# Kernel optimization log

Measured on AMD Instinct MI355X. Metric: run time of the kernel, lower is better.

Reference implementation:

```python
import jax, jax.numpy as jnp
import numpy as np
from functools import partial

B, S, T = 32, 64, 64
VS, VT = 32000, 32000
E, H = 256, 512            # embed_dim, encoder hidden per direction
DH = 2 * H                 # decoder hidden (= encoder_hidden_dim)
A = 128                    # attention_dim


def _p(key, shape, scale=0.05):
    return scale * jax.random.normal(key, shape, dtype=jnp.float32)


def setup_inputs() -> dict:
    key = jax.random.key(0)
    ks = jax.random.split(key, 32)
    inp = {
        'src': jax.random.randint(ks[0], (B, S), 0, VS),
        'tgt_input': jax.random.randint(ks[1], (B, T), 0, VT),
        # encoder
        'enc_emb': _p(ks[2], (VS, E)),
        'enc_Wih_f': _p(ks[3], (4 * H, E)), 'enc_Whh_f': _p(ks[4], (4 * H, H)),
        'enc_bih_f': _p(ks[5], (4 * H,)),  'enc_bhh_f': _p(ks[6], (4 * H,)),
        'enc_Wih_b': _p(ks[7], (4 * H, E)), 'enc_Whh_b': _p(ks[8], (4 * H, H)),
        'enc_bih_b': _p(ks[9], (4 * H,)),  'enc_bhh_b': _p(ks[10], (4 * H,)),
        # decoder
        'dec_emb': _p(ks[11], (VT, E)),
        'Wd': _p(ks[12], (A, DH)), 'bd': _p(ks[13], (A,)),
        'We': _p(ks[14], (A, DH)), 'be': _p(ks[15], (A,)),
        'v_att': _p(ks[16], (A,)), 'bv': _p(ks[17], ()),
        'dec_Wih': _p(ks[18], (4 * DH, E + DH)), 'dec_Whh': _p(ks[19], (4 * DH, DH)),
        'dec_bih': _p(ks[20], (4 * DH,)), 'dec_bhh': _p(ks[21], (4 * DH,)),
        'Wo': _p(ks[22], (VT, DH + DH)), 'bo': _p(ks[23], (VT,)),
    }
    return inp


def _lstm_cell(x, h, c, Wih, Whh, b):
    g = x @ Wih.T + h @ Whh.T + b
    i, f, gg, o = jnp.split(g, 4, axis=-1)  # PyTorch gate order: i,f,g,o
    i, f, o = jax.nn.sigmoid(i), jax.nn.sigmoid(f), jax.nn.sigmoid(o)
    c_new = f * c + i * jnp.tanh(gg)
    h_new = o * jnp.tanh(c_new)
    return h_new, c_new


def _lstm_scan(xs, Wih, Whh, b, reverse):
    # xs: [S,B,E] -> outputs [S,B,H] aligned with input positions, final (h,c)
    h0 = jnp.zeros((xs.shape[1], Whh.shape[1]), xs.dtype)
    def step(carry, x):
        h, c = carry
        h, c = _lstm_cell(x, h, c, Wih, Whh, b)
        return (h, c), h
    (hT, cT), hs = jax.lax.scan(step, (h0, h0), xs, reverse=reverse)
    return hs, hT, cT


def _forward(src, tgt_input, enc_emb,
             enc_Wih_f, enc_Whh_f, enc_bih_f, enc_bhh_f,
             enc_Wih_b, enc_Whh_b, enc_bih_b, enc_bhh_b,
             dec_emb, Wd, bd, We, be, v_att, bv,
             dec_Wih, dec_Whh, dec_bih, dec_bhh, Wo, bo):
    # ---- Encoder: bidirectional single-layer LSTM ----
    emb = enc_emb[src]                              # [B,S,E]
    xs = emb.transpose(1, 0, 2)                     # [S,B,E]
    hs_f, hT_f, cT_f = _lstm_scan(xs, enc_Wih_f, enc_Whh_f, enc_bih_f + enc_bhh_f, False)
    hs_b, hT_b, cT_b = _lstm_scan(xs, enc_Wih_b, enc_Whh_b, enc_bih_b + enc_bhh_b, True)
    enc_out = jnp.concatenate([hs_f, hs_b], axis=-1).transpose(1, 0, 2)  # [B,S,2H]
    h = jnp.concatenate([hT_f, hT_b], axis=-1)      # [B,DH]
    c = jnp.concatenate([cT_f, cT_b], axis=-1)

    # ---- Decoder with Bahdanau attention (full teacher forcing) ----
    enc_proj = enc_out @ We.T + be                  # [B,S,A] precomputed
    dec_b = dec_bih + dec_bhh
    tgt_emb = dec_emb[tgt_input].transpose(1, 0, 2)  # [T,B,E]

    def dec_step(carry, emb_t):
        h, c = carry
        dproj = h @ Wd.T + bd                       # [B,A]
        energy = jnp.tanh(dproj[:, None, :] + enc_proj)  # [B,S,A]
        scores = energy @ v_att + bv                # [B,S]
        w = jax.nn.softmax(scores, axis=1)
        ctx = jnp.einsum('bs,bsh->bh', w, enc_out)  # [B,DH]
        x = jnp.concatenate([emb_t, ctx], axis=-1)  # [B,E+DH]
        h_new, c_new = _lstm_cell(x, h, c, dec_Wih, dec_Whh, dec_b)
        logits = jnp.concatenate([h_new, ctx], axis=-1) @ Wo.T + bo  # [B,VT]
        return (h_new, c_new), logits

    _, logits = jax.lax.scan(dec_step, (h, c), tgt_emb)  # [T,B,VT]
    return logits.transpose(1, 0, 2)                     # [B,T,VT]


def reference(src, tgt_input, enc_emb,
              enc_Wih_f, enc_Whh_f, enc_bih_f, enc_bhh_f,
              enc_Wih_b, enc_Whh_b, enc_bih_b, enc_bhh_b,
              dec_emb, Wd, bd, We, be, v_att, bv,
              dec_Wih, dec_Whh, dec_bih, dec_bhh, Wo, bo):
    return _forward(src, tgt_input, enc_emb,
                    enc_Wih_f, enc_Whh_f, enc_bih_f, enc_bhh_f,
                    enc_Wih_b, enc_Whh_b, enc_bih_b, enc_bhh_b,
                    dec_emb, Wd, bd, We, be, v_att, bv,
                    dec_Wih, dec_Whh, dec_bih, dec_bhh, Wo, bo)
```

## Files before the change

### kernel.cpp

```cpp
#include <hip/hip_runtime.h>


using u16 = unsigned short;
using u32 = unsigned int;
using u64 = unsigned long long;
using f32x4 = __attribute__((ext_vector_type(4))) float;
using s16x8 = __attribute__((ext_vector_type(8))) short;
using u16x4 = __attribute__((ext_vector_type(4))) unsigned short;

__device__ __forceinline__ float sigm_(float x) { return 1.0f / (1.0f + expf(-x)); }
__device__ __forceinline__ float tanh_(float x) {
    float e = __expf(fminf(2.0f * x, 30.0f));
    return (e - 1.0f) / (e + 1.0f);
}

__device__ __forceinline__ u16 f2bf(float x) {
    u32 u = __float_as_uint(x);
    u += 0x7fffu + ((u >> 16) & 1u);
    return (u16)(u >> 16);
}
__device__ __forceinline__ u32 pk2(float a, float b) {
    return (u32)f2bf(a) | ((u32)f2bf(b) << 16);
}
__device__ __forceinline__ float bf2f(u16 v) {
    return __uint_as_float((u32)v << 16);
}

__device__ __forceinline__ void ast32(u32* p, u32 v) {
    __hip_atomic_store(p, v, __ATOMIC_RELAXED, __HIP_MEMORY_SCOPE_AGENT);
}

#define MFMA __builtin_amdgcn_mfma_f32_16x16x32_bf16

#define GLL(g, l) __builtin_amdgcn_global_load_lds( \
    (__attribute__((address_space(1))) void*)(g),   \
    (__attribute__((address_space(3))) void*)(l), 16, 0, 0)

__device__ __forceinline__ void poll8(const int* go8) {
    if (threadIdx.x < 8) {
        const int* p = go8 + threadIdx.x * 16;
        while (__hip_atomic_load(p, __ATOMIC_RELAXED, __HIP_MEMORY_SCOPE_AGENT) == 0)
            __builtin_amdgcn_s_sleep(1);
    }
    __syncthreads();
    asm volatile("" ::: "memory");
}
__device__ __forceinline__ void arrive8(int* cnt8, int* go8, int line, int perline) {
    asm volatile("s_waitcnt vmcnt(0) lgkmcnt(0)" ::: "memory");
    __syncthreads();
    if (threadIdx.x == 0) {
        int old = __hip_atomic_fetch_add(cnt8 + line * 16, 1, __ATOMIC_RELAXED,
                                         __HIP_MEMORY_SCOPE_AGENT);
        if (old == perline - 1)
            __hip_atomic_store(go8 + line * 16, 1, __ATOMIC_RELAXED, __HIP_MEMORY_SCOPE_AGENT);
    }
}

__global__ __launch_bounds__(256) void k_zero(float* __restrict__ p, int n) {
    int i = blockIdx.x * 256 + threadIdx.x;
    if (i < n) p[i] = 0.0f;
}

__global__ __launch_bounds__(256) void k_cast_bf16(const float* __restrict__ in,
                                                   u16* __restrict__ outp, int n8) {
    int idx = blockIdx.x * 256 + threadIdx.x;
    if (idx >= n8) return;
    const f32x4* p = (const f32x4*)in + (size_t)idx * 2;
    f32x4 a = p[0], c = p[1];
    u32* o = (u32*)(outp + (size_t)idx * 8);
    o[0] = pk2(a.x, a.y); o[1] = pk2(a.z, a.w);
    o[2] = pk2(c.x, c.y); o[3] = pk2(c.z, c.w);
}

__global__ __launch_bounds__(256) void k_embed_bf(const int* __restrict__ tok,
                                                  const float* __restrict__ emb,
                                                  u16* __restrict__ outp) {
    int idx = blockIdx.x * 256 + threadIdx.x;
    int r = idx >> 6, e4 = idx & 63;
    int outer = r >> 5, b = r & 31;
    int tk = tok[b * 64 + outer];
    f32x4 v = ((const f32x4*)emb)[(size_t)tk * 64 + e4];
    u32* o = (u32*)(outp + (size_t)r * 256 + (e4 << 2));
    o[0] = pk2(v.x, v.y); o[1] = pk2(v.z, v.w);
}

__global__ __launch_bounds__(256) void k_prep_perm(
    const float* __restrict__ src, u16* __restrict__ dst,
    int J, int K4, int srcStride, int srcOff, int total)
{
    int idx = blockIdx.x * 256 + threadIdx.x;
    if (idx >= total) return;
    int n = idx / K4, kq = (idx - n * K4) << 2;
    int orig = (n & 3) * J + (n >> 2);
    f32x4 v = *(const f32x4*)(src + (size_t)orig * srcStride + srcOff + kq);
    u32* o = (u32*)(dst + (size_t)n * (K4 << 2) + kq);
    o[0] = pk2(v.x, v.y); o[1] = pk2(v.z, v.w);
}

__global__ __launch_bounds__(256) void k_prep_ws(
    const float* __restrict__ W, u16* __restrict__ dst)
{
    int idx = blockIdx.x * 256 + threadIdx.x;
    int n = idx >> 8, kp = idx & 255, k0 = kp << 1;
    int orig = (n & 3) * 512 + (n >> 2);
    const float* s = W + (size_t)orig * 512 + k0;
    int g = n >> 5, r = n & 31;
    int byteoff = (k0 << 1) ^ ((r & 7) << 4);
    *(u32*)((char*)dst + (size_t)g * 32768 + r * 1024 + byteoff) = pk2(s[0], s[1]);
}

__global__ __launch_bounds__(256) void k_prep_w2s(
    const float* __restrict__ Whh, const float* __restrict__ Wih, u16* __restrict__ dst)
{
    int idx = blockIdx.x * 256 + threadIdx.x;
    int n = idx >> 10, kp = idx & 1023, k0 = kp << 1;
    int orig = (n & 3) * 1024 + (n >> 2);
    const float* s = (k0 < 1024) ? (Whh + (size_t)orig * 1024 + k0)
                                 : (Wih + (size_t)orig * 1280 + 256 + (k0 - 1024));
    int g = n >> 5, r = n & 31;
    int byteoff = (k0 << 1) ^ ((r & 7) << 4);
    *(u32*)((char*)dst + (size_t)g * 131072 + r * 4096 + byteoff) = pk2(s[0], s[1]);
}

__global__ __launch_bounds__(256) void k_gemm_bf(
    const u16* __restrict__ A, const u16* __restrict__ B, int K,
    const float* __restrict__ b1, const float* __restrict__ b2, int biasJ,
    float* __restrict__ C, int ldc, int nM, int nN, int remapOut, int swz)
{
    __shared__ __align__(16) u16 As[128 * 32];
    __shared__ __align__(16) u16 Bs[128 * 32];
    int w = blockIdx.x;
    if (swz) { int cpx = (nM * nN) >> 3; w = (w & 7) * cpx + (w >> 3); }
    int bm = (w % nM) * 128, bn = (w / nM) * 128;
    int tid = threadIdx.x, wave = tid >> 6, lane = tid & 63;
    int wm = wave & 1, wn = wave >> 1;
    f32x4 acc[4][4] = {};

    int rA = wave * 32 + (lane >> 2);
    int cb2 = (lane & 3) * 16;
    const char* gA = (const char*)A + ((size_t)(bm + rA) * K) * 2 + cb2;
    const char* gB = (const char*)B + ((size_t)(bn + rA) * K) * 2 + cb2;
    size_t rowskip = (size_t)16 * K * 2;
    char* lA = (char*)As + wave * 2048;
    char* lB = (char*)Bs + wave * 2048;
    const u16* rdA = As + (wm * 64 + (lane & 15)) * 32 + (lane >> 4) * 8;
    const u16* rdB = Bs + (wn * 64 + (lane & 15)) * 32 + (lane >> 4) * 8;

    for (int k0 = 0; k0 < K; k0 += 32) {
        size_t kb = (size_t)k0 * 2;
        GLL(gA + kb, lA); GLL(gA + kb + rowskip, lA + 1024);
        GLL(gB + kb, lB); GLL(gB + kb + rowskip, lB + 1024);
        __syncthreads();
        s16x8 af[4], bfv[4];
#pragma unroll
        for (int m2 = 0; m2 < 4; ++m2) af[m2] = *(const s16x8*)(rdA + m2 * 512);
#pragma unroll
        for (int n2 = 0; n2 < 4; ++n2) bfv[n2] = *(const s16x8*)(rdB + n2 * 512);
#pragma unroll
        for (int m2 = 0; m2 < 4; ++m2)
#pragma unroll
            for (int n2 = 0; n2 < 4; ++n2)
                acc[m2][n2] = MFMA(af[m2], bfv[n2], acc[m2][n2], 0, 0, 0);
        __syncthreads();
    }

    int rbase = bm + wm * 64 + ((lane >> 4) << 2);
    int cbase = bn + wn * 64 + (lane & 15);
#pragma unroll
    for (int n2 = 0; n2 < 4; ++n2) {
        int col = cbase + n2 * 16;
        int bcol = biasJ ? ((col & 3) * biasJ + (col >> 2)) : col;
        float bias = (b1 ? b1[bcol] : 0.0f) + (b2 ? b2[bcol] : 0.0f);
#pragma unroll
        for (int m2 = 0; m2 < 4; ++m2) {
            f32x4 v = acc[m2][n2];
#pragma unroll
            for (int jj = 0; jj < 4; ++jj) {
                int row = rbase + m2 * 16 + jj;
                int orow = remapOut ? ((row & 31) * 64 + (row >> 5)) : row;
                C[(size_t)orow * ldc + col] = v[jj] + bias;
            }
        }
    }
}

__global__ __launch_bounds__(256, 1) void k_enc_persist(
    const u16* __restrict__ Wsf, const u16* __restrict__ Wsb,
    const float* __restrict__ Gfp, const float* __restrict__ Gbp,
    u16* __restrict__ henc,
    float* __restrict__ cfb,
    u16* __restrict__ encbf,
    int* __restrict__ cnt8, int* __restrict__ go8)
{
    __shared__ __align__(16) char smem[50176];
    int tid = threadIdx.x, lane = tid & 63, q = tid >> 6;
    int dir = blockIdx.x >> 6, g = blockIdx.x & 63;
    const char* wsrc = (const char*)(dir ? Wsb : Wsf) + (size_t)g * 32768;
#pragma unroll
    for (int it = 0; it < 8; ++it)
        GLL(wsrc + it * 4096 + tid * 16, smem + it * 4096 + tid * 16);
    __syncthreads();

    float* sacc = (float*)(smem + 32768);
    u16* hst = (u16*)(smem + 49664);
    const float* Gp = dir ? Gbp : Gfp;
    float* cB = cfb + dir * 16384;
    int lr = lane & 15, lk = (lane >> 4) << 3;
    int bb = tid & 31, jl = tid >> 5;
    int n0 = g * 32, j = g * 8 + jl;

    for (int s = 0; s < 64; ++s) {
        if (s) poll8(go8 + s * 128);
        int t = dir ? (63 - s) : s;
        f32x4 p4 = *(const f32x4*)(Gp + ((size_t)(t * 32 + bb)) * 2048 + n0 + (jl << 2));
        const u16* hA = henc + (size_t)s * 32768 + dir * 16384;
        s16x8 afr[8];
#pragma unroll
        for (int it = 0; it < 4; ++it) {
            int ke = q * 128 + it * 32 + lk;
            afr[2 * it]     = *(const s16x8*)(hA + lr * 512 + ke);
            afr[2 * it + 1] = *(const s16x8*)(hA + (lr + 16) * 512 + ke);
        }
        f32x4 acc00 = {}, acc01 = {}, acc10 = {}, acc11 = {};
#pragma unroll
        for (int it = 0; it < 4; ++it) {
            int ke = q * 128 + it * 32 + lk;
            int kb = ke << 1;
            s16x8 b0 = *(const s16x8*)(smem + lr * 1024 + (kb ^ ((lr & 7) << 4)));
            int r1 = lr + 16;
            s16x8 b1 = *(const s16x8*)(smem + r1 * 1024 + (kb ^ ((r1 & 7) << 4)));
            acc00 = MFMA(afr[2 * it], b0, acc00, 0, 0, 0);
            acc01 = MFMA(afr[2 * it], b1, acc01, 0, 0, 0);
            acc10 = MFMA(afr[2 * it + 1], b0, acc10, 0, 0, 0);
            acc11 = MFMA(afr[2 * it + 1], b1, acc11, 0, 0, 0);
        }
        int rw = (lane >> 4) << 2;
#pragma unroll
        for (int rr = 0; rr < 4; ++rr) {
            sacc[q * 1056 + (rw + rr) * 33 + lr]        = acc00[rr];
            sacc[q * 1056 + (rw + rr) * 33 + 16 + lr]   = acc01[rr];
            sacc[q * 1056 + (16 + rw + rr) * 33 + lr]      = acc10[rr];
            sacc[q * 1056 + (16 + rw + rr) * 33 + 16 + lr] = acc11[rr];
        }
        __syncthreads();
        {
            int c4 = jl << 2;
            float gi = 0, gf = 0, gg = 0, go2 = 0;
#pragma unroll
            for (int q2 = 0; q2 < 4; ++q2) {
                const float* sp = sacc + q2 * 1056 + bb * 33 + c4;
                gi += sp[0]; gf += sp[1]; gg += sp[2]; go2 += sp[3];
            }
            gi += p4.x; gf += p4.y; gg += p4.z; go2 += p4.w;
            float* cp = cB + bb * 512 + j;
            float cn = sigm_(gf) * cp[0] + sigm_(gi) * tanhf(gg);
            cp[0] = cn;
            float h = sigm_(go2) * tanhf(cn);
            u16 h16 = f2bf(h);
            encbf[((size_t)(bb * 64 + t)) * 1024 + dir * 512 + j] = h16;
            hst[bb * 8 + jl] = h16;
        }
        __syncthreads();
        if (tid < 128) {
            int bb2 = tid >> 2, p2 = tid & 3;
            u32 wv = (u32)hst[bb2 * 8 + 2 * p2] | ((u32)hst[bb2 * 8 + 2 * p2 + 1] << 16);
            ast32((u32*)(henc + (size_t)(s + 1) * 32768 + dir * 16384) + bb2 * 256 + g * 4 + p2, wv);
        }
        arrive8(cnt8 + (s + 1) * 128, go8 + (s + 1) * 128, blockIdx.x & 7, 16);
    }
}

__global__ __launch_bounds__(256) void k_dec_init(
    const u16* __restrict__ henc, const float* __restrict__ cfb,
    u16* __restrict__ hcarr, float* __restrict__ cd)
{
    int idx = blockIdx.x * 256 + threadIdx.x;
    int b = idx >> 10, j = idx & 1023;
    int dir = (j >> 9), jj = j & 511;
    hcarr[b * 2048 + j] = henc[(size_t)64 * 32768 + dir * 16384 + b * 512 + jj];
    cd[b * 1024 + j] = cfb[dir * 16384 + b * 512 + jj];
}

__global__ __launch_bounds__(256, 1) void k_dec_persist(
    const u16* __restrict__ W2s, const u16* __restrict__ encbf,
    const float* __restrict__ Prep,
    const u16* __restrict__ Wd_bf, const float* __restrict__ bd,
    const float* __restrict__ eproj, const float* __restrict__ v_att,
    const float* __restrict__ bv,
    u16* __restrict__ hcarr, float* __restrict__ cd, u16* __restrict__ Abf,
    const u16* __restrict__ Wbf, const float* __restrict__ bo,
    float* __restrict__ outp,
    int* __restrict__ hCnt8, int* __restrict__ goH8,
    int* __restrict__ ctxCnt8, int* __restrict__ goCtx8)
{
    __shared__ __align__(16) char smem[148480];
    int blk = blockIdx.x, tid = threadIdx.x, lane = tid & 63, q = tid >> 6;

    if (blk >= 160) {
        int w = blk - 160;
        u16* As = (u16*)smem;
        u16* Bs = (u16*)(smem + 8192);
        int wave = q, wm = wave & 1, wn = wave >> 1;
        int rA = wave * 32 + (lane >> 2);
        int cb2 = (lane & 3) * 16;
        size_t rowskip = (size_t)16 * 2048 * 2;
        char* lA = (char*)As + wave * 2048;
        char* lB = (char*)Bs + wave * 2048;
        const u16* rdA = As + (wm * 64 + (lane & 15)) * 32 + (lane >> 4) * 8;
        const u16* rdB = Bs + (wn * 64 + (lane & 15)) * 32 + (lane >> 4) * 8;
        for (int g = 0; g < 16; ++g) {
            poll8(goH8 + (4 * g + 4) * 128);
            int bm = g * 128;
            const char* gA = (const char*)Abf + ((size_t)(bm + rA) * 2048) * 2 + cb2;
            for (int nt = w; nt < 250; nt += 96) {
                int bn = nt * 128;
                const char* gB = (const char*)Wbf + ((size_t)(bn + rA) * 2048) * 2 + cb2;
                f32x4 acc[4][4] = {};
                for (int k0 = 0; k0 < 2048; k0 += 32) {
                    size_t kb = (size_t)k0 * 2;
                    GLL(gA + kb, lA); GLL(gA + kb + rowskip, lA + 1024);
                    GLL(gB + kb, lB); GLL(gB + kb + rowskip, lB + 1024);
                    __syncthreads();
                    s16x8 af[4], bfv[4];
#pragma unroll
                    for (int m2 = 0; m2 < 4; ++m2) af[m2] = *(const s16x8*)(rdA + m2 * 512);
#pragma unroll
                    for (int n2 = 0; n2 < 4; ++n2) bfv[n2] = *(const s16x8*)(rdB + n2 * 512);
#pragma unroll
                    for (int m2 = 0; m2 < 4; ++m2)
#pragma unroll
                        for (int n2 = 0; n2 < 4; ++n2)
                            acc[m2][n2] = MFMA(af[m2], bfv[n2], acc[m2][n2], 0, 0, 0);
                    __syncthreads();
                }
                int rbase = bm + wm * 64 + ((lane >> 4) << 2);
                int cbase = bn + wn * 64 + (lane & 15);
#pragma unroll
                for (int n2 = 0; n2 < 4; ++n2) {
                    int col = cbase + n2 * 16;
                    float bias = bo[col];
#pragma unroll
                    for (int m2 = 0; m2 < 4; ++m2) {
                        f32x4 v = acc[m2][n2];
#pragma unroll
                        for (int jj = 0; jj < 4; ++jj) {
                            int row = rbase + m2 * 16 + jj;
                            int orow = (row & 31) * 64 + (row >> 5);
                            outp[(size_t)orow * 32000 + col] = v[jj] + bias;
                        }
                    }
                }
            }
        }
        return;
    }

    bool isgate = blk < 128;
    {
        const char* src = isgate ? ((const char*)W2s + (size_t)blk * 131072)
                                 : ((const char*)encbf + (size_t)(blk - 128) * 131072);
#pragma unroll
        for (int it = 0; it < 32; ++it)
            GLL(src + it * 4096 + tid * 16, smem + it * 4096 + tid * 16);
    }
    __syncthreads();

    float* sacc = (float*)(smem + 131072);
    u16* hst    = (u16*)(smem + 147968);
    float* hsh  = (float*)(smem + 131072);
    float* red  = (float*)(smem + 135168);
    float* dp   = (float*)(smem + 136192);
    float* sc   = (float*)(smem + 136704);

    int lr = lane & 15, lk = (lane >> 4) << 3;
    int bb = tid & 31, jl = tid >> 5;
    int n0 = blk * 32, j = blk * 8 + jl;
    int b = blk - 128;

    for (int t = 0; t < 64; ++t) {
        if (t) poll8(goH8 + t * 128);
        const u16* hcT = hcarr + (size_t)t * 65536;
        if (isgate) {
            f32x4 p4 = *(const f32x4*)(Prep + ((size_t)(t * 32 + bb)) * 4096 + n0 + (jl << 2));
            s16x8 afr[16];
#pragma unroll
            for (int it = 0; it < 8; ++it) {
                int ke = q * 256 + it * 32 + lk;
                afr[2 * it]     = *(const s16x8*)(hcT + lr * 2048 + ke);
                afr[2 * it + 1] = *(const s16x8*)(hcT + (lr + 16) * 2048 + ke);
            }
            f32x4 acc00 = {}, acc01 = {}, acc10 = {}, acc11 = {};
#pragma unroll
            for (int it = 0; it < 8; ++it) {
                int ke = q * 256 + it * 32 + lk;
                int kb = ke << 1;
                s16x8 b0 = *(const s16x8*)(smem + lr * 4096 + (kb ^ ((lr & 7) << 4)));
                int r1 = lr + 16;
                s16x8 b1 = *(const s16x8*)(smem + r1 * 4096 + (kb ^ ((r1 & 7) << 4)));
                acc00 = MFMA(afr[2 * it], b0, acc00, 0, 0, 0);
                acc01 = MFMA(afr[2 * it], b1, acc01, 0, 0, 0);
                acc10 = MFMA(afr[2 * it + 1], b0, acc10, 0, 0, 0);
                acc11 = MFMA(afr[2 * it + 1], b1, acc11, 0, 0, 0);
            }
            poll8(goCtx8 + t * 128);
#pragma unroll
            for (int it = 0; it < 8; ++it) {
                int ke = 1024 + q * 256 + it * 32 + lk;
                afr[2 * it]     = *(const s16x8*)(hcT + lr * 2048 + ke);
                afr[2 * it + 1] = *(const s16x8*)(hcT + (lr + 16) * 2048 + ke);
            }
#pragma unroll
            for (int it = 0; it < 8; ++it) {
                int ke = 1024 + q * 256 + it * 32 + lk;
                int kb = ke << 1;
                s16x8 b0 = *(const s16x8*)(smem + lr * 4096 + (kb ^ ((lr & 7) << 4)));
                int r1 = lr + 16;
                s16x8 b1 = *(const s16x8*)(smem + r1 * 4096 + (kb ^ ((r1 & 7) << 4)));
                acc00 = MFMA(afr[2 * it], b0, acc00, 0, 0, 0);
                acc01 = MFMA(afr[2 * it], b1, acc01, 0, 0, 0);
                acc10 = MFMA(afr[2 * it + 1], b0, acc10, 0, 0, 0);
                acc11 = MFMA(afr[2 * it + 1], b1, acc11, 0, 0, 0);
            }
            int rw = (lane >> 4) << 2;
#pragma unroll
            for (int rr = 0; rr < 4; ++rr) {
                sacc[q * 1056 + (rw + rr) * 33 + lr]        = acc00[rr];
                sacc[q * 1056 + (rw + rr) * 33 + 16 + lr]   = acc01[rr];
                sacc[q * 1056 + (16 + rw + rr) * 33 + lr]      = acc10[rr];
                sacc[q * 1056 + (16 + rw + rr) * 33 + 16 + lr] = acc11[rr];
            }
            __syncthreads();
            {
                int c4 = jl << 2;
                float gi = 0, gf = 0, gg = 0, go2 = 0;
#pragma unroll
                for (int q2 = 0; q2 < 4; ++q2) {
                    const float* sp = sacc + q2 * 1056 + bb * 33 + c4;
                    gi += sp[0]; gf += sp[1]; gg += sp[2]; go2 += sp[3];
                }
                gi += p4.x; gf += p4.y; gg += p4.z; go2 += p4.w;
                int ci = bb * 1024 + j;
                float cn = sigm_(gf) * cd[ci] + sigm_(gi) * tanhf(gg);
                cd[ci] = cn;
                float h = sigm_(go2) * tanhf(cn);
                hst[bb * 8 + jl] = f2bf(h);
            }
            __syncthreads();
            if (tid < 128) {
                int bb2 = tid >> 2, p2 = tid & 3;
                u32 wv = (u32)hst[bb2 * 8 + 2 * p2] | ((u32)hst[bb2 * 8 + 2 * p2 + 1] << 16);
                ast32((u32*)(hcarr + (size_t)(t + 1) * 65536) + bb2 * 1024 + blk * 4 + p2, wv);
                ast32((u32*)Abf + (size_t)(t * 32 + bb2) * 1024 + blk * 4 + p2, wv);
            }
            arrive8(hCnt8 + (t + 1) * 128, goH8 + (t + 1) * 128, blk & 7, 16);
        } else {
            {
                u16x4 hv = *(const u16x4*)(hcT + b * 2048 + (tid << 2));
                hsh[(tid << 2) + 0] = bf2f(hv.x);
                hsh[(tid << 2) + 1] = bf2f(hv.y);
                hsh[(tid << 2) + 2] = bf2f(hv.z);
                hsh[(tid << 2) + 3] = bf2f(hv.w);
            }
            __syncthreads();
            {
                int a = tid & 127, half = tid >> 7;
                const u16* wr = Wd_bf + ((size_t)a << 10) + (half << 9);
                const float* hh = hsh + (half << 9);
                float s0 = 0, s1 = 0, s2 = 0, s3 = 0;
#pragma unroll 4
                for (int k = 0; k < 512; k += 32) {
                    s16x8 w0 = *(const s16x8*)(wr + k);
                    s16x8 w1 = *(const s16x8*)(wr + k + 8);
                    s16x8 w2 = *(const s16x8*)(wr + k + 16);
                    s16x8 w3 = *(const s16x8*)(wr + k + 24);
#pragma unroll
                    for (int e = 0; e < 8; ++e) {
                        s0 += bf2f((u16)w0[e]) * hh[k + e];
                        s1 += bf2f((u16)w1[e]) * hh[k + 8 + e];
                        s2 += bf2f((u16)w2[e]) * hh[k + 16 + e];
                        s3 += bf2f((u16)w3[e]) * hh[k + 24 + e];
                    }
                }
                red[tid] = (s0 + s1) + (s2 + s3);
            }
            __syncthreads();
            if (tid < 128) dp[tid] = red[tid] + red[tid + 128] + bd[tid];
            __syncthreads();
            {
                int si = tid >> 2, qq = tid & 3;
                const float* ep = eproj + ((size_t)(b * 64 + si)) * 128 + qq * 32;
                float s = 0.0f;
#pragma unroll 8
                for (int a2 = 0; a2 < 32; ++a2)
                    s += v_att[qq * 32 + a2] * tanh_(dp[qq * 32 + a2] + ep[a2]);
                red[tid] = s;
            }
            __syncthreads();
            if (tid < 64) {
                float x = red[tid * 4] + red[tid * 4 + 1] + red[tid * 4 + 2] + red[tid * 4 + 3] + bv[0];
                float mx = x;
#pragma unroll
                for (int off = 32; off; off >>= 1) mx = fmaxf(mx, __shfl_xor(mx, off));
                float e = __expf(x - mx), ss = e;
#pragma unroll
                for (int off = 32; off; off >>= 1) ss += __shfl_xor(ss, off);
                sc[tid] = e / ss;
            }
            __syncthreads();
            {
                const u16* eL = (const u16*)smem;
                int c0i = tid << 2;
                float c0 = 0, c1 = 0, c2 = 0, c3 = 0;
                for (int s2 = 0; s2 < 64; ++s2) {
                    float wgt = sc[s2];
                    u16x4 rp = *(const u16x4*)(eL + s2 * 1024 + c0i);
                    c0 += wgt * bf2f(rp.x); c1 += wgt * bf2f(rp.y);
                    c2 += wgt * bf2f(rp.z); c3 += wgt * bf2f(rp.w);
                }
                u32 cw0 = pk2(c0, c1), cw1 = pk2(c2, c3);
                u32* hw = (u32*)hcT + b * 1024 + 512 + (tid << 1);
                ast32(hw, cw0); ast32(hw + 1, cw1);
                u32* aw = (u32*)(Abf + ((size_t)(t * 32 + b)) * 2048 + 1024 + c0i);
                ast32(aw, cw0); ast32(aw + 1, cw1);
            }
            arrive8(ctxCnt8 + t * 128, goCtx8 + t * 128, blk & 7, 4);
        }
    }
}

extern "C" void kernel_launch(void* const* d_in, const int* in_sizes, int n_in,
                              void* d_out, int out_size, void* d_ws, size_t ws_size,
                              hipStream_t stream)
{
    (void)in_sizes; (void)n_in; (void)out_size; (void)ws_size;
    const int*   src     = (const int*)d_in[0];
    const int*   tgt     = (const int*)d_in[1];
    const float* enc_emb = (const float*)d_in[2];
    const float* eWih_f  = (const float*)d_in[3];
    const float* eWhh_f  = (const float*)d_in[4];
    const float* ebih_f  = (const float*)d_in[5];
    const float* ebhh_f  = (const float*)d_in[6];
    const float* eWih_b  = (const float*)d_in[7];
    const float* eWhh_b  = (const float*)d_in[8];
    const float* ebih_b  = (const float*)d_in[9];
    const float* ebhh_b  = (const float*)d_in[10];
    const float* dec_emb = (const float*)d_in[11];
    const float* Wd      = (const float*)d_in[12];
    const float* bd      = (const float*)d_in[13];
    const float* We      = (const float*)d_in[14];
    const float* be      = (const float*)d_in[15];
    const float* v_att   = (const float*)d_in[16];
    const float* bv      = (const float*)d_in[17];
    const float* dWih    = (const float*)d_in[18];
    const float* dWhh    = (const float*)d_in[19];
    const float* dbih    = (const float*)d_in[20];
    const float* dbhh    = (const float*)d_in[21];
    const float* Wo      = (const float*)d_in[22];
    const float* bo      = (const float*)d_in[23];
    float* out = (float*)d_out;

    char* wp = (char*)d_ws;
    auto alloc = [&](size_t nbytes) -> void* {
        void* p = (void*)wp;
        wp += (nbytes + 255) & ~(size_t)255;
        return p;
    };
    u16*   Xe_bf = (u16*)alloc(2048u * 256 * 2);
    u16*   Ed_bf = (u16*)alloc(2048u * 256 * 2);
    float* Gf_p  = (float*)alloc(2048u * 2048 * 4);
    float* Gb_p  = (float*)alloc(2048u * 2048 * 4);
    float* Pre_p = (float*)alloc(2048u * 4096 * 4);
    float* zr    = (float*)alloc(329728u);
    float* cfb   = zr;
    char*  sy    = (char*)zr + 131072;
    int*   cntE8 = (int*)(sy);
    int*   goE8  = (int*)(sy + 33280);
    int*   hCnt8 = (int*)(sy + 66560);
    int*   goH8  = (int*)(sy + 99840);
    int*   ctxC8 = (int*)(sy + 133120);
    int*   goX8  = (int*)(sy + 165888);
    u16*   henc  = (u16*)alloc(65u * 32768 * 2);
    u16*   hcarr = (u16*)alloc(65u * 65536 * 2);
    u16*   encbf = (u16*)alloc(2048u * 1024 * 2);
    float* eproj = (float*)alloc(2048u * 128 * 4);
    float* cd    = (float*)alloc(32768u * 4);
    u16*   Abf   = (u16*)alloc(2048u * 2048 * 2);
    u16*   Wbf   = (u16*)alloc(32000u * 2048 * 2);
    u16*   W2s   = (u16*)alloc(4096u * 2048 * 2);
    u16*   Wsf   = (u16*)alloc(2048u * 512 * 2);
    u16*   Wsb   = (u16*)alloc(2048u * 512 * 2);
    u16*   Wembf = (u16*)alloc(2048u * 256 * 2);
    u16*   Wembb = (u16*)alloc(2048u * 256 * 2);
    u16*   Wembd = (u16*)alloc(4096u * 256 * 2);
    u16*   We_bf = (u16*)alloc(128u * 1024 * 2);
    u16*   Wd_bf = (u16*)alloc(128u * 1024 * 2);

    k_zero<<<322, 256, 0, stream>>>(zr, 82432);
    k_zero<<<64, 256, 0, stream>>>((float*)henc, 16384);

    k_cast_bf16<<<32000, 256, 0, stream>>>(Wo, Wbf, 8192000);
    k_cast_bf16<<<64, 256, 0, stream>>>(We, We_bf, 16384);
    k_cast_bf16<<<64, 256, 0, stream>>>(Wd, Wd_bf, 16384);
    k_prep_perm<<<512, 256, 0, stream>>>(eWih_f, Wembf, 512, 64, 256, 0, 131072);
    k_prep_perm<<<512, 256, 0, stream>>>(eWih_b, Wembb, 512, 64, 256, 0, 131072);
    k_prep_perm<<<1024, 256, 0, stream>>>(dWih, Wembd, 1024, 64, 1280, 0, 262144);
    k_prep_ws<<<2048, 256, 0, stream>>>(eWhh_f, Wsf);
    k_prep_ws<<<2048, 256, 0, stream>>>(eWhh_b, Wsb);
    k_prep_w2s<<<16384, 256, 0, stream>>>(dWhh, dWih, W2s);

    k_embed_bf<<<512, 256, 0, stream>>>(src, enc_emb, Xe_bf);
    k_embed_bf<<<512, 256, 0, stream>>>(tgt, dec_emb, Ed_bf);

    k_gemm_bf<<<256, 256, 0, stream>>>(Xe_bf, Wembf, 256, ebih_f, ebhh_f, 512,
                                       Gf_p, 2048, 16, 16, 0, 1);
    k_gemm_bf<<<256, 256, 0, stream>>>(Xe_bf, Wembb, 256, ebih_b, ebhh_b, 512,
                                       Gb_p, 2048, 16, 16, 0, 1);
    k_gemm_bf<<<512, 256, 0, stream>>>(Ed_bf, Wembd, 256, dbih, dbhh, 1024,
                                       Pre_p, 4096, 16, 32, 0, 1);

    k_enc_persist<<<128, 256, 0, stream>>>(Wsf, Wsb, Gf_p, Gb_p, henc, cfb, encbf,
                                           cntE8, goE8);

    k_gemm_bf<<<16, 256, 0, stream>>>(encbf, We_bf, 1024, be, nullptr, 0,
                                      eproj, 128, 16, 1, 0, 1);
    k_dec_init<<<128, 256, 0, stream>>>(henc, cfb, hcarr, cd);

    k_dec_persist<<<256, 256, 0, stream>>>(W2s, encbf, Pre_p, Wd_bf, bd, eproj,
                                           v_att, bv, hcarr, cd, Abf,
                                           Wbf, bo, out,
                                           hCnt8, goH8, ctxC8, goX8);
}
```

Measured before the change: 2.280 ms.

## Overlap weight bf16 casts with encoder recurrence and batch output GEMM per 256 rows

After: 2.272 ms. No clear change (-0.3%).

```diff
diff --git a/kernel.cpp b/kernel.cpp
--- a/kernel.cpp
+++ b/kernel.cpp
@@ -59,17 +59,6 @@
 __global__ __launch_bounds__(256) void k_zero(float* __restrict__ p, int n) {
     int i = blockIdx.x * 256 + threadIdx.x;
     if (i < n) p[i] = 0.0f;
-}
-
-__global__ __launch_bounds__(256) void k_cast_bf16(const float* __restrict__ in,
-                                                   u16* __restrict__ outp, int n8) {
-    int idx = blockIdx.x * 256 + threadIdx.x;
-    if (idx >= n8) return;
-    const f32x4* p = (const f32x4*)in + (size_t)idx * 2;
-    f32x4 a = p[0], c = p[1];
-    u32* o = (u32*)(outp + (size_t)idx * 8);
-    o[0] = pk2(a.x, a.y); o[1] = pk2(a.z, a.w);
-    o[2] = pk2(c.x, c.y); o[3] = pk2(c.z, c.w);
 }
 
 __global__ __launch_bounds__(256) void k_embed_bf(const int* __restrict__ tok,
@@ -107,19 +96,6 @@
     int g = n >> 5, r = n & 31;
     int byteoff = (k0 << 1) ^ ((r & 7) << 4);
     *(u32*)((char*)dst + (size_t)g * 32768 + r * 1024 + byteoff) = pk2(s[0], s[1]);
-}
-
-__global__ __launch_bounds__(256) void k_prep_w2s(
-    const float* __restrict__ Whh, const float* __restrict__ Wih, u16* __restrict__ dst)
-{
-    int idx = blockIdx.x * 256 + threadIdx.x;
-    int n = idx >> 10, kp = idx & 1023, k0 = kp << 1;
-    int orig = (n & 3) * 1024 + (n >> 2);
-    const float* s = (k0 < 1024) ? (Whh + (size_t)orig * 1024 + k0)
-                                 : (Wih + (size_t)orig * 1280 + 256 + (k0 - 1024));
-    int g = n >> 5, r = n & 31;
-    int byteoff = (k0 << 1) ^ ((r & 7) << 4);
-    *(u32*)((char*)dst + (size_t)g * 131072 + r * 4096 + byteoff) = pk2(s[0], s[1]);
 }
 
 __global__ __launch_bounds__(256) void k_gemm_bf(
@@ -190,10 +166,49 @@
     u16* __restrict__ henc,
     float* __restrict__ cfb,
     u16* __restrict__ encbf,
-    int* __restrict__ cnt8, int* __restrict__ go8)
+    int* __restrict__ cnt8, int* __restrict__ go8,
+    const float* __restrict__ Wo, u16* __restrict__ Wbf,
+    const float* __restrict__ We, u16* __restrict__ We_bf,
+    const float* __restrict__ Wd, u16* __restrict__ Wd_bf,
+    const float* __restrict__ dWhh, const float* __restrict__ dWih,
+    u16* __restrict__ W2s)
 {
     __shared__ __align__(16) char smem[50176];
     int tid = threadIdx.x, lane = tid & 63, q = tid >> 6;
+
+    if (blockIdx.x >= 128) {
+        int gt = (blockIdx.x - 128) * 256 + tid;
+        for (int i = gt; i < 8192000; i += 32768) {
+            const f32x4* p = (const f32x4*)Wo + (size_t)i * 2;
+            f32x4 a = p[0], c = p[1];
+            u32* o = (u32*)(Wbf + (size_t)i * 8);
+            o[0] = pk2(a.x, a.y); o[1] = pk2(a.z, a.w);
+            o[2] = pk2(c.x, c.y); o[3] = pk2(c.z, c.w);
+        }
+        if (gt < 16384) {
+            const f32x4* p = (const f32x4*)We + (size_t)gt * 2;
+            f32x4 a = p[0], c = p[1];
+            u32* o = (u32*)(We_bf + (size_t)gt * 8);
+            o[0] = pk2(a.x, a.y); o[1] = pk2(a.z, a.w);
+            o[2] = pk2(c.x, c.y); o[3] = pk2(c.z, c.w);
+            const f32x4* p2 = (const f32x4*)Wd + (size_t)gt * 2;
+            f32x4 a2 = p2[0], c2 = p2[1];
+            u32* o2 = (u32*)(Wd_bf + (size_t)gt * 8);
+            o2[0] = pk2(a2.x, a2.y); o2[1] = pk2(a2.z, a2.w);
+            o2[2] = pk2(c2.x, c2.y); o2[3] = pk2(c2.z, c2.w);
+        }
+        for (int i = gt; i < 4194304; i += 32768) {
+            int n = i >> 10, kp = i & 1023, k0 = kp << 1;
+            int orig = (n & 3) * 1024 + (n >> 2);
+            const float* s = (k0 < 1024) ? (dWhh + (size_t)orig * 1024 + k0)
+                                         : (dWih + (size_t)orig * 1280 + 256 + (k0 - 1024));
+            int g2 = n >> 5, r = n & 31;
+            int byteoff = (k0 << 1) ^ ((r & 7) << 4);
+            *(u32*)((char*)W2s + (size_t)g2 * 131072 + r * 4096 + byteoff) = pk2(s[0], s[1]);
+        }
+        return;
+    }
+
     int dir = blockIdx.x >> 6, g = blockIdx.x & 63;
     const char* wsrc = (const char*)(dir ? Wsb : Wsf) + (size_t)g * 32768;
 #pragma unroll
@@ -300,53 +315,55 @@
         int w = blk - 160;
         u16* As = (u16*)smem;
         u16* Bs = (u16*)(smem + 8192);
-        int wave = q, wm = wave & 1, wn = wave >> 1;
-        int rA = wave * 32 + (lane >> 2);
+        int wm = q & 1, wn = q >> 1;
+        int rA = q * 32 + (lane >> 2);
         int cb2 = (lane & 3) * 16;
         size_t rowskip = (size_t)16 * 2048 * 2;
-        char* lA = (char*)As + wave * 2048;
-        char* lB = (char*)Bs + wave * 2048;
+        char* lA = (char*)As + q * 2048;
+        char* lB = (char*)Bs + q * 2048;
         const u16* rdA = As + (wm * 64 + (lane & 15)) * 32 + (lane >> 4) * 8;
         const u16* rdB = Bs + (wn * 64 + (lane & 15)) * 32 + (lane >> 4) * 8;
-        for (int g = 0; g < 16; ++g) {
-            poll8(goH8 + (4 * g + 4) * 128);
-            int bm = g * 128;
-            const char* gA = (const char*)Abf + ((size_t)(bm + rA) * 2048) * 2 + cb2;
+        for (int g = 0; g < 8; ++g) {
+            poll8(goH8 + (8 * (g + 1)) * 128);
             for (int nt = w; nt < 250; nt += 96) {
                 int bn = nt * 128;
                 const char* gB = (const char*)Wbf + ((size_t)(bn + rA) * 2048) * 2 + cb2;
-                f32x4 acc[4][4] = {};
-                for (int k0 = 0; k0 < 2048; k0 += 32) {
-                    size_t kb = (size_t)k0 * 2;
-                    GLL(gA + kb, lA); GLL(gA + kb + rowskip, lA + 1024);
-                    GLL(gB + kb, lB); GLL(gB + kb + rowskip, lB + 1024);
-                    __syncthreads();
-                    s16x8 af[4], bfv[4];
-#pragma unroll
-                    for (int m2 = 0; m2 < 4; ++m2) af[m2] = *(const s16x8*)(rdA + m2 * 512);
-#pragma unroll
-                    for (int n2 = 0; n2 < 4; ++n2) bfv[n2] = *(const s16x8*)(rdB + n2 * 512);
-#pragma unroll
-                    for (int m2 = 0; m2 < 4; ++m2)
-#pragma unroll
-                        for (int n2 = 0; n2 < 4; ++n2)
-                            acc[m2][n2] = MFMA(af[m2], bfv[n2], acc[m2][n2], 0, 0, 0);
-                    __syncthreads();
-                }
-                int rbase = bm + wm * 64 + ((lane >> 4) << 2);
-                int cbase = bn + wn * 64 + (lane & 15);
-#pragma unroll
-                for (int n2 = 0; n2 < 4; ++n2) {
-                    int col = cbase + n2 * 16;
-                    float bias = bo[col];
-#pragma unroll
-                    for (int m2 = 0; m2 < 4; ++m2) {
-                        f32x4 v = acc[m2][n2];
-#pragma unroll
-                        for (int jj = 0; jj < 4; ++jj) {
-                            int row = rbase + m2 * 16 + jj;
-                            int orow = (row & 31) * 64 + (row >> 5);
-                            outp[(size_t)orow * 32000 + col] = v[jj] + bias;
+                for (int mt = 0; mt < 2; ++mt) {
+                    int bm = g * 256 + mt * 128;
+                    const char* gA = (const char*)Abf + ((size_t)(bm + rA) * 2048) * 2 + cb2;
+                    f32x4 acc[4][4] = {};
+                    for (int k0 = 0; k0 < 2048; k0 += 32) {
+                        size_t kb = (size_t)k0 * 2;
+                        GLL(gA + kb, lA); GLL(gA + kb + rowskip, lA + 1024);
+                        GLL(gB + kb, lB); GLL(gB + kb + rowskip, lB + 1024);
+                        __syncthreads();
+                        s16x8 af[4], bfv[4];
+#pragma unroll
+                        for (int m2 = 0; m2 < 4; ++m2) af[m2] = *(const s16x8*)(rdA + m2 * 512);
+#pragma unroll
+                        for (int n2 = 0; n2 < 4; ++n2) bfv[n2] = *(const s16x8*)(rdB + n2 * 512);
+#pragma unroll
+                        for (int m2 = 0; m2 < 4; ++m2)
+#pragma unroll
+                            for (int n2 = 0; n2 < 4; ++n2)
+                                acc[m2][n2] = MFMA(af[m2], bfv[n2], acc[m2][n2], 0, 0, 0);
+                        __syncthreads();
+                    }
+                    int rbase = bm + wm * 64 + ((lane >> 4) << 2);
+                    int cbase = bn + wn * 64 + (lane & 15);
+#pragma unroll
+                    for (int n2 = 0; n2 < 4; ++n2) {
+                        int col = cbase + n2 * 16;
+                        float bias = bo[col];
+#pragma unroll
+                        for (int m2 = 0; m2 < 4; ++m2) {
+                            f32x4 v = acc[m2][n2];
+#pragma unroll
+                            for (int jj = 0; jj < 4; ++jj) {
+                                int row = rbase + m2 * 16 + jj;
+                                int orow = (row & 31) * 64 + (row >> 5);
+                                outp[(size_t)orow * 32000 + col] = v[jj] + bias;
+                            }
                         }
                     }
                 }
@@ -598,15 +615,11 @@
     k_zero<<<322, 256, 0, stream>>>(zr, 82432);
     k_zero<<<64, 256, 0, stream>>>((float*)henc, 16384);
 
-    k_cast_bf16<<<32000, 256, 0, stream>>>(Wo, Wbf, 8192000);
-    k_cast_bf16<<<64, 256, 0, stream>>>(We, We_bf, 16384);
-    k_cast_bf16<<<64, 256, 0, stream>>>(Wd, Wd_bf, 16384);
     k_prep_perm<<<512, 256, 0, stream>>>(eWih_f, Wembf, 512, 64, 256, 0, 131072);
     k_prep_perm<<<512, 256, 0, stream>>>(eWih_b, Wembb, 512, 64, 256, 0, 131072);
     k_prep_perm<<<1024, 256, 0, stream>>>(dWih, Wembd, 1024, 64, 1280, 0, 262144);
     k_prep_ws<<<2048, 256, 0, stream>>>(eWhh_f, Wsf);
     k_prep_ws<<<2048, 256, 0, stream>>>(eWhh_b, Wsb);
-    k_prep_w2s<<<16384, 256, 0, stream>>>(dWhh, dWih, W2s);
 
     k_embed_bf<<<512, 256, 0, stream>>>(src, enc_emb, Xe_bf);
     k_embed_bf<<<512, 256, 0, stream>>>(tgt, dec_emb, Ed_bf);
@@ -618,8 +631,10 @@
     k_gemm_bf<<<512, 256, 0, stream>>>(Ed_bf, Wembd, 256, dbih, dbhh, 1024,
                                        Pre_p, 4096, 16, 32, 0, 1);
 
-    k_enc_persist<<<128, 256, 0, stream>>>(Wsf, Wsb, Gf_p, Gb_p, henc, cfb, encbf,
-                                           cntE8, goE8);
+    k_enc_persist<<<256, 256, 0, stream>>>(Wsf, Wsb, Gf_p, Gb_p, henc, cfb, encbf,
+                                           cntE8, goE8,
+                                           Wo, Wbf, We, We_bf, Wd, Wd_bf,
+                                           dWhh, dWih, W2s);
 
     k_gemm_bf<<<16, 256, 0, stream>>>(encbf, We_bf, 1024, be, nullptr, 0,
                                       eproj, 128, 16, 1, 0, 1);
```
